# Optimization experiments

Hardware: AMD Instinct MI355X
Metric: run time of the kernel (lower is better)

Reference implementation:

```python
import jax, jax.numpy as jnp
import numpy as np
import math

H_SP, W_SP = 200, 200          # BEV spatial shape (single level, m == h)
D_MODEL = 256
N_HEADS = 8
N_POINTS = 4
D_HEAD = D_MODEL // N_HEADS


def _grid_init_bias():
    # Matches TemporalSelfAttention._reset_parameters for sampling_offsets.bias
    thetas = np.arange(N_HEADS, dtype=np.float32) * (2.0 * np.pi / N_HEADS)
    grid = np.stack([np.cos(thetas), np.sin(thetas)], -1)
    grid = grid / np.abs(grid).max(-1, keepdims=True)
    grid = np.tile(grid[:, None, None, :], (1, 1, N_POINTS, 1))  # (NH, 1, P, 2)
    for i in range(N_POINTS):
        grid[:, :, i, :] *= (i + 1)
    return jnp.asarray(grid.reshape(-1), dtype=jnp.float32)


def setup_inputs() -> dict:
    key = jax.random.key(0)
    ks = jax.random.split(key, 10)
    N = 1
    Lq = H_SP * W_SP
    Lin = H_SP * W_SP
    xav = math.sqrt(6.0 / (2 * D_MODEL))
    query = jax.random.normal(ks[0], (N, Lq, D_MODEL), jnp.float32)
    query_pos = jax.random.normal(ks[1], (N, Lq, D_MODEL), jnp.float32)
    reference_points = jax.random.uniform(ks[2], (N, Lq, 1, 2), jnp.float32)
    input_flatten = jax.random.normal(ks[3], (N, Lin, D_MODEL), jnp.float32)
    W_value = jax.random.uniform(ks[4], (D_MODEL, D_MODEL), jnp.float32, -xav, xav)
    b_value = jnp.zeros((D_MODEL,), jnp.float32)
    # small random weights (trained-model-like) + canonical grid bias
    W_off = jax.random.normal(ks[5], (N_HEADS * N_POINTS * 2, D_MODEL), jnp.float32) * 0.005
    b_off = _grid_init_bias()
    W_attn = jax.random.normal(ks[6], (N_HEADS * N_POINTS, D_MODEL), jnp.float32) * 0.02
    b_attn = jnp.zeros((N_HEADS * N_POINTS,), jnp.float32)
    W_out = jax.random.uniform(ks[7], (D_MODEL, D_MODEL), jnp.float32, -xav, xav)
    b_out = jnp.zeros((D_MODEL,), jnp.float32)
    return dict(query=query, query_pos=query_pos, reference_points=reference_points,
                input_flatten=input_flatten, W_value=W_value, b_value=b_value,
                W_off=W_off, b_off=b_off, W_attn=W_attn, b_attn=b_attn,
                W_out=W_out, b_out=b_out)


def _bilinear_sample(vflat, x, y):
    # vflat: (N, NH, H*W, DH); x, y: (N, NH, K) pixel coords (align_corners=False)
    # Zero padding outside the feature map, matching the MSDeformAttn CUDA kernel.
    x0f = jnp.floor(x)
    y0f = jnp.floor(y)
    x0 = x0f.astype(jnp.int32)
    y0 = y0f.astype(jnp.int32)
    lw = x - x0f
    lh = y - y0f
    gather = jax.vmap(jax.vmap(lambda v, i: v[i]))  # over batch, head
    acc = jnp.zeros(x.shape + (vflat.shape[-1],), vflat.dtype)
    corners = ((y0, x0, (1.0 - lh) * (1.0 - lw)),
               (y0, x0 + 1, (1.0 - lh) * lw),
               (y0 + 1, x0, lh * (1.0 - lw)),
               (y0 + 1, x0 + 1, lh * lw))
    for yi, xi, wgt in corners:
        valid = ((xi >= 0) & (xi < W_SP) & (yi >= 0) & (yi < H_SP)).astype(vflat.dtype)
        idx = jnp.clip(yi, 0, H_SP - 1) * W_SP + jnp.clip(xi, 0, W_SP - 1)
        g = gather(vflat, idx)                      # (N, NH, K, DH)
        acc = acc + (wgt * valid)[..., None] * g
    return acc


def reference(query, query_pos, reference_points, input_flatten,
              W_value, b_value, W_off, b_off, W_attn, b_attn, W_out, b_out):
    N, Lq, _ = query.shape
    q = query + query_pos
    value = input_flatten @ W_value.T + b_value                     # (N, Lin, D)
    value = value.reshape(N, -1, N_HEADS, D_HEAD).transpose(0, 2, 1, 3)  # (N, NH, Lin, DH)
    off = (q @ W_off.T + b_off).reshape(N, Lq, N_HEADS, N_POINTS, 2)
    attn = jax.nn.softmax((q @ W_attn.T + b_attn).reshape(N, Lq, N_HEADS, N_POINTS), axis=-1)
    norm = jnp.array([W_SP, H_SP], jnp.float32)                      # offset_normalizer (w, h)
    ref = reference_points[:, :, 0, :][:, :, None, None, :]          # (N, Lq, 1, 1, 2)
    loc = ref + off / norm                                           # (N, Lq, NH, P, 2) in [0,1]
    x = (loc[..., 0] * W_SP - 0.5).transpose(0, 2, 1, 3).reshape(N, N_HEADS, Lq * N_POINTS)
    y = (loc[..., 1] * H_SP - 0.5).transpose(0, 2, 1, 3).reshape(N, N_HEADS, Lq * N_POINTS)
    sampled = _bilinear_sample(value, x, y).reshape(N, N_HEADS, Lq, N_POINTS, D_HEAD)
    out = jnp.einsum('nhqpd,nqhp->nqhd', sampled, attn).reshape(N, Lq, D_MODEL)
    return out @ W_out.T + b_out
```

## Files before the change

kernel.cpp:

```cpp
#include <hip/hip_runtime.h>
#include <math.h>

#define LQ 40000
#define DMODEL 256
#define NHD 8
#define NPT 4
#define DHD 32
#define HSP 200
#define WSP 200
#define NSTRIP (LQ / 16)
#define G1B 128
#define G2B 256

typedef short s16x8 __attribute__((ext_vector_type(8)));
typedef float f32x4 __attribute__((ext_vector_type(4)));

__device__ __forceinline__ unsigned short f2b(float f) {
    unsigned u = __builtin_bit_cast(unsigned, f);
    u += 0x7FFFu + ((u >> 16) & 1u);
    return (unsigned short)(u >> 16);
}
__device__ __forceinline__ float b2f(unsigned short u) {
    return __builtin_bit_cast(float, ((unsigned)u) << 16);
}
__device__ __forceinline__ void pk8(const float4& v0, const float4& v1,
                                    unsigned short* o) {
    o[0] = f2b(v0.x); o[1] = f2b(v0.y); o[2] = f2b(v0.z); o[3] = f2b(v0.w);
    o[4] = f2b(v1.x); o[5] = f2b(v1.y); o[6] = f2b(v1.z); o[7] = f2b(v1.w);
}


__global__ __launch_bounds__(256) void convert_weights(
    const float* __restrict__ Wv, const float* __restrict__ Woff,
    const float* __restrict__ Wattn, const float* __restrict__ Wout,
    unsigned short* __restrict__ dst)
{
    int u = blockIdx.x * 256 + threadIdx.x;
    int lane = u & 63, ks = (u >> 6) & 7, slot = u >> 9;
    int l15 = lane & 15, quad = lane >> 4;
    const float* src;
    if (slot < 16) {
        src = Wv + (size_t)(slot * 16 + l15) * 256;
    } else if (slot < 22) {
        int col = (slot - 16) * 16 + l15;
        src = (col < 64) ? Woff + (size_t)col * 256
                         : Wattn + (size_t)(col - 64) * 256;
    } else {
        src = Wout + (size_t)((slot - 22) * 16 + l15) * 256;
    }
    int k0 = ks * 32 + quad * 8;
    float4 v0 = *(const float4*)(src + k0);
    float4 v1 = *(const float4*)(src + k0 + 4);
    union { unsigned short u16[8]; uint4 v; } tmp;
    pk8(v0, v1, tmp.u16);
    *(uint4*)(dst + (size_t)u * 8) = tmp.v;
}


__global__ __launch_bounds__(256, 2) void gemm12(
    const float* __restrict__ input_flatten,
    const float* __restrict__ query, const float* __restrict__ query_pos,
    const unsigned short* __restrict__ wf,
    const float* __restrict__ bv, const float* __restrict__ boff,
    const float* __restrict__ battn,
    unsigned short* __restrict__ val, float* __restrict__ raw2)
{
    __shared__ unsigned short Blds[32768];

    const int bid = blockIdx.x;
    const int t = threadIdx.x;
    const int role = (bid < 2 * G1B) ? 0 : 1;
    const int half8 = (bid >= G1B && role == 0) ? 1 : 0;

    {
        const uint4* src = (const uint4*)(wf + (role ? 16 : half8 * 8) * 4096);
        const int nu = role ? 3072 : 4096;
        for (int i = t; i < nu; i += 256) ((uint4*)Blds)[i] = src[i];
    }
    __syncthreads();

    const int wave = t >> 6, lane = t & 63;
    const int l15 = lane & 15, quad = lane >> 4;

    if (role == 0) {
        float bias[8];
#pragma unroll
        for (int c = 0; c < 8; ++c) bias[c] = bv[(half8 * 8 + c) * 16 + l15];
        const int wgid = (bid - half8 * G1B) * 4 + wave;
        for (int g = wgid; g < NSTRIP; g += G1B * 4) {
            const float* base = input_flatten + ((size_t)g * 16 + l15) * 256;
            float4 p0[8], p1[8];
#pragma unroll
            for (int ks = 0; ks < 8; ++ks) {
                p0[ks] = *(const float4*)(base + ks * 32 + quad * 8);
                p1[ks] = *(const float4*)(base + ks * 32 + quad * 8 + 4);
            }
            asm volatile("" ::: "memory");
            s16x8 a[8];
#pragma unroll
            for (int ks = 0; ks < 8; ++ks) {
                union { unsigned short u16[8]; s16x8 v; } tmp;
                pk8(p0[ks], p1[ks], tmp.u16);
                a[ks] = tmp.v;
            }
#pragma unroll
            for (int c = 0; c < 8; ++c) {
                const int gc = half8 * 8 + c;
                f32x4 acc = (f32x4){0.f, 0.f, 0.f, 0.f};
#pragma unroll
                for (int ks = 0; ks < 8; ++ks)
                    acc = __builtin_amdgcn_mfma_f32_16x16x32_bf16(
                        a[ks], *(const s16x8*)&Blds[c * 4096 + ks * 512 + lane * 8],
                        acc, 0, 0, 0);
#pragma unroll
                for (int r2 = 0; r2 < 4; ++r2) {
                    size_t row = (size_t)g * 16 + quad * 4 + r2;
                    val[(((size_t)(gc >> 1) * LQ + row) << 5) + ((gc & 1) << 4) + l15]
                        = f2b(acc[r2] + bias[c]);
                }
            }
        }
    } else {
        float bias[6];
#pragma unroll
        for (int c = 0; c < 6; ++c) {
            int col = c * 16 + l15;
            bias[c] = (col < 64) ? boff[col] : battn[col - 64];
        }
        const int wgid = (bid - 2 * G1B) * 4 + wave;
        for (int g = wgid; g < NSTRIP; g += G2B * 4) {
            const float* base  = query     + ((size_t)g * 16 + l15) * 256;
            const float* base2 = query_pos + ((size_t)g * 16 + l15) * 256;
            float4 p0[8], p1[8], q0[8], q1[8];
#pragma unroll
            for (int ks = 0; ks < 8; ++ks) {
                p0[ks] = *(const float4*)(base + ks * 32 + quad * 8);
                p1[ks] = *(const float4*)(base + ks * 32 + quad * 8 + 4);
                q0[ks] = *(const float4*)(base2 + ks * 32 + quad * 8);
                q1[ks] = *(const float4*)(base2 + ks * 32 + quad * 8 + 4);
            }
            asm volatile("" ::: "memory");
            s16x8 a[8];
#pragma unroll
            for (int ks = 0; ks < 8; ++ks) {
                float4 v0 = p0[ks], v1 = p1[ks];
                v0.x += q0[ks].x; v0.y += q0[ks].y;
                v0.z += q0[ks].z; v0.w += q0[ks].w;
                v1.x += q1[ks].x; v1.y += q1[ks].y;
                v1.z += q1[ks].z; v1.w += q1[ks].w;
                union { unsigned short u16[8]; s16x8 v; } tmp;
                pk8(v0, v1, tmp.u16);
                a[ks] = tmp.v;
            }
#pragma unroll
            for (int c = 0; c < 6; ++c) {
                f32x4 acc = (f32x4){0.f, 0.f, 0.f, 0.f};
#pragma unroll
                for (int ks = 0; ks < 8; ++ks)
                    acc = __builtin_amdgcn_mfma_f32_16x16x32_bf16(
                        a[ks], *(const s16x8*)&Blds[c * 4096 + ks * 512 + lane * 8],
                        acc, 0, 0, 0);
#pragma unroll
                for (int r2 = 0; r2 < 4; ++r2) {
                    size_t row = (size_t)g * 16 + quad * 4 + r2;
                    float v = acc[r2] + bias[c];
                    int col = c * 16 + l15;
                    int hh, jj;
                    if (col < 64) { hh = col >> 3; jj = col & 7; }
                    else          { hh = (col - 64) >> 2; jj = 8 + (col & 3); }
                    raw2[((size_t)hh * LQ + row) * 12 + jj] = v;
                }
            }
        }
    }
}

__global__ __launch_bounds__(256, 2) void gemm4(
    const unsigned short* __restrict__ Af, const unsigned short* __restrict__ wf,
    const float* __restrict__ bout, float* __restrict__ C)
{
    __shared__ unsigned short Blds[32768];

    const int t = threadIdx.x;
    const int half8 = blockIdx.x >> 7;
    {
        const uint4* src = (const uint4*)(wf + (22 + half8 * 8) * 4096);
        for (int i = t; i < 4096; i += 256) ((uint4*)Blds)[i] = src[i];
    }
    __syncthreads();

    const int wave = t >> 6, lane = t & 63;
    const int l15 = lane & 15, quad = lane >> 4;

    float bias[8];
#pragma unroll
    for (int c = 0; c < 8; ++c) bias[c] = bout[(half8 * 8 + c) * 16 + l15];

    const int wgid = (blockIdx.x & 127) * 4 + wave;
    for (int g = wgid; g < NSTRIP; g += 128 * 4) {
        s16x8 a[8];
#pragma unroll
        for (int ks = 0; ks < 8; ++ks)
            a[ks] = *(const s16x8*)&Af[(size_t)g * 4096 + ks * 512 + lane * 8];
        asm volatile("" ::: "memory");
#pragma unroll
        for (int c = 0; c < 8; ++c) {
            const int gc = half8 * 8 + c;
            f32x4 acc = (f32x4){0.f, 0.f, 0.f, 0.f};
#pragma unroll
            for (int ks = 0; ks < 8; ++ks)
                acc = __builtin_amdgcn_mfma_f32_16x16x32_bf16(
                    a[ks], *(const s16x8*)&Blds[c * 4096 + ks * 512 + lane * 8],
                    acc, 0, 0, 0);
#pragma unroll
            for (int r2 = 0; r2 < 4; ++r2) {
                size_t row = (size_t)g * 16 + quad * 4 + r2;
                C[row * 256 + gc * 16 + l15] = acc[r2] + bias[c];
            }
        }
    }
}

__global__ __launch_bounds__(256) void sample_kernel(
    const float* __restrict__ raw2, const float* __restrict__ rp,
    const unsigned short* __restrict__ value, unsigned short* __restrict__ outa)
{
    __shared__ int4   sIdx[64][4];
    __shared__ float4 sW[64][4];

    const int h = blockIdx.x & 7;
    const int q0 = (blockIdx.x >> 3) * 64;
    const int t = threadIdx.x;
    {
        const int qi = t >> 2, p = t & 3;
        const int q = q0 + qi;
        const float* r = raw2 + ((size_t)h * LQ + q) * 12;
        float l0 = r[8], l1 = r[9], l2 = r[10], l3 = r[11];
        float mx = fmaxf(fmaxf(l0, l1), fmaxf(l2, l3));
        float e0 = __expf(l0 - mx), e1 = __expf(l1 - mx);
        float e2 = __expf(l2 - mx), e3 = __expf(l3 - mx);
        float inv = 1.f / (e0 + e1 + e2 + e3);
        float ep = (p == 0) ? e0 : (p == 1) ? e1 : (p == 2) ? e2 : e3;
        float wp = ep * inv;

        float x = rp[(size_t)q * 2 + 0] * (float)WSP - 0.5f + r[p * 2 + 0];
        float y = rp[(size_t)q * 2 + 1] * (float)HSP - 0.5f + r[p * 2 + 1];
        float x0f = floorf(x), y0f = floorf(y);
        int x0 = (int)x0f, y0 = (int)y0f;
        float lw = x - x0f, lh = y - y0f;
        float cw[4] = {(1.f - lh) * (1.f - lw), (1.f - lh) * lw,
                       lh * (1.f - lw), lh * lw};
        int4 I; float4 W;
        int* Ip = &I.x; float* Wp = &W.x;
#pragma unroll
        for (int c = 0; c < 4; ++c) {
            int cx = x0 + (c & 1), cy = y0 + (c >> 1);
            bool valid = (cx >= 0) & (cx < WSP) & (cy >= 0) & (cy < HSP);
            int ccx = cx < 0 ? 0 : (cx > WSP - 1 ? WSP - 1 : cx);
            int ccy = cy < 0 ? 0 : (cy > HSP - 1 ? HSP - 1 : cy);
            Ip[c] = (ccy * WSP + ccx) * DHD;
            Wp[c] = valid ? cw[c] * wp : 0.f;
        }
        sIdx[qi][p] = I;
        sW[qi][p] = W;
    }
    __syncthreads();

    const int d8 = t & 7, qp = t >> 3;
    const unsigned short* vp = value + (size_t)h * LQ * DHD + d8 * 4;
#pragma unroll
    for (int e = 0; e < 2; ++e) {
        int qi = qp * 2 + e;
        float a0 = 0.f, a1 = 0.f, a2 = 0.f, a3 = 0.f;
#pragma unroll
        for (int p = 0; p < 4; ++p) {
            int4 I = sIdx[qi][p];
            float4 W = sW[qi][p];
            uint2 g0 = *(const uint2*)(vp + I.x);
            uint2 g1 = *(const uint2*)(vp + I.y);
            uint2 g2 = *(const uint2*)(vp + I.z);
            uint2 g3 = *(const uint2*)(vp + I.w);
            a0 += W.x * b2f((unsigned short)g0.x);
            a1 += W.x * b2f((unsigned short)(g0.x >> 16));
            a2 += W.x * b2f((unsigned short)g0.y);
            a3 += W.x * b2f((unsigned short)(g0.y >> 16));
            a0 += W.y * b2f((unsigned short)g1.x);
            a1 += W.y * b2f((unsigned short)(g1.x >> 16));
            a2 += W.y * b2f((unsigned short)g1.y);
            a3 += W.y * b2f((unsigned short)(g1.y >> 16));
            a0 += W.z * b2f((unsigned short)g2.x);
            a1 += W.z * b2f((unsigned short)(g2.x >> 16));
            a2 += W.z * b2f((unsigned short)g2.y);
            a3 += W.z * b2f((unsigned short)(g2.y >> 16));
            a0 += W.w * b2f((unsigned short)g3.x);
            a1 += W.w * b2f((unsigned short)(g3.x >> 16));
            a2 += W.w * b2f((unsigned short)g3.y);
            a3 += W.w * b2f((unsigned short)(g3.y >> 16));
        }
        int q = q0 + qi;
        size_t off = (size_t)(q >> 4) * 4096 + h * 512 + (d8 >> 1) * 128
                   + (q & 15) * 8 + (d8 & 1) * 4;
        union { unsigned short u16[4]; uint2 v; } o;
        o.u16[0] = f2b(a0); o.u16[1] = f2b(a1);
        o.u16[2] = f2b(a2); o.u16[3] = f2b(a3);
        *(uint2*)&outa[off] = o.v;
    }
}

extern "C" void kernel_launch(void* const* d_in, const int* in_sizes, int n_in,
                              void* d_out, int out_size, void* d_ws, size_t ws_size,
                              hipStream_t stream)
{
    const float* query         = (const float*)d_in[0];
    const float* query_pos     = (const float*)d_in[1];
    const float* ref_points    = (const float*)d_in[2];
    const float* input_flatten = (const float*)d_in[3];
    const float* W_value       = (const float*)d_in[4];
    const float* b_value       = (const float*)d_in[5];
    const float* W_off         = (const float*)d_in[6];
    const float* b_off         = (const float*)d_in[7];
    const float* W_attn        = (const float*)d_in[8];
    const float* b_attn        = (const float*)d_in[9];
    const float* W_out         = (const float*)d_in[10];
    const float* b_out         = (const float*)d_in[11];
    float* out = (float*)d_out;

    unsigned short* val  = (unsigned short*)d_ws;
    float*          raw2 = (float*)(val + (size_t)LQ * DMODEL);
    unsigned short* outa = (unsigned short*)(raw2 + (size_t)LQ * 96);
    unsigned short* wf   = outa + (size_t)LQ * DMODEL;

    dim3 blk(256);

    convert_weights<<<dim3(76), blk, 0, stream>>>(W_value, W_off, W_attn, W_out, wf);

    gemm12<<<dim3(2 * G1B + G2B), blk, 0, stream>>>(
        input_flatten, query, query_pos, wf,
        b_value, b_off, b_attn, val, raw2);

    sample_kernel<<<dim3(8 * (LQ / 64)), blk, 0, stream>>>(raw2, ref_points, val, outa);

    gemm4<<<dim3(256), blk, 0, stream>>>(outa, wf, b_out, out);
}
```

Before: 236.2 us.

## Use 1024-thread one-strip-per-wave blocks for projection GEMMs, dropping grid-stride loops

The value/offset/attention GEMM and the output GEMM now launch 1024-thread blocks, each wave handling exactly one 16-row strip instead of grid-striding over strips. This lets each block's LDS weight tile be shared by 16 waves and exposes more parallel waves to hide global-load latency. The query+query_pos loads in the second role are split into two halves to cut register pressure. In exchange, each block pays a larger weight-staging cost relative to its work, and the last blocks are partly idle.

```diff
diff --git a/kernel.cpp b/kernel.cpp
--- a/kernel.cpp
+++ b/kernel.cpp
@@ -9,8 +9,7 @@
 #define HSP 200
 #define WSP 200
 #define NSTRIP (LQ / 16)
-#define G1B 128
-#define G2B 256
+#define B1 157
 
 typedef short s16x8 __attribute__((ext_vector_type(8)));
 typedef float f32x4 __attribute__((ext_vector_type(4)));
@@ -57,7 +56,7 @@
 }
 
 
-__global__ __launch_bounds__(256, 2) void gemm12(
+__global__ __launch_bounds__(1024, 4) void gemm12(
     const float* __restrict__ input_flatten,
     const float* __restrict__ query, const float* __restrict__ query_pos,
     const unsigned short* __restrict__ wf,
@@ -69,13 +68,13 @@
 
     const int bid = blockIdx.x;
     const int t = threadIdx.x;
-    const int role = (bid < 2 * G1B) ? 0 : 1;
-    const int half8 = (bid >= G1B && role == 0) ? 1 : 0;
+    const int role = (bid < 2 * B1) ? 0 : 1;
+    const int half8 = (role == 0 && bid >= B1) ? 1 : 0;
 
     {
         const uint4* src = (const uint4*)(wf + (role ? 16 : half8 * 8) * 4096);
         const int nu = role ? 3072 : 4096;
-        for (int i = t; i < nu; i += 256) ((uint4*)Blds)[i] = src[i];
+        for (int i = t; i < nu; i += 1024) ((uint4*)Blds)[i] = src[i];
     }
     __syncthreads();
 
@@ -83,126 +82,26 @@
     const int l15 = lane & 15, quad = lane >> 4;
 
     if (role == 0) {
+        const int g = (bid - half8 * B1) * 16 + wave;
+        if (g >= NSTRIP) return;
         float bias[8];
 #pragma unroll
         for (int c = 0; c < 8; ++c) bias[c] = bv[(half8 * 8 + c) * 16 + l15];
-        const int wgid = (bid - half8 * G1B) * 4 + wave;
-        for (int g = wgid; g < NSTRIP; g += G1B * 4) {
-            const float* base = input_flatten + ((size_t)g * 16 + l15) * 256;
-            float4 p0[8], p1[8];
-#pragma unroll
-            for (int ks = 0; ks < 8; ++ks) {
-                p0[ks] = *(const float4*)(base + ks * 32 + quad * 8);
-                p1[ks] = *(const float4*)(base + ks * 32 + quad * 8 + 4);
-            }
-            asm volatile("" ::: "memory");
-            s16x8 a[8];
-#pragma unroll
-            for (int ks = 0; ks < 8; ++ks) {
-                union { unsigned short u16[8]; s16x8 v; } tmp;
-                pk8(p0[ks], p1[ks], tmp.u16);
-                a[ks] = tmp.v;
-            }
-#pragma unroll
-            for (int c = 0; c < 8; ++c) {
-                const int gc = half8 * 8 + c;
-                f32x4 acc = (f32x4){0.f, 0.f, 0.f, 0.f};
-#pragma unroll
-                for (int ks = 0; ks < 8; ++ks)
-                    acc = __builtin_amdgcn_mfma_f32_16x16x32_bf16(
-                        a[ks], *(const s16x8*)&Blds[c * 4096 + ks * 512 + lane * 8],
-                        acc, 0, 0, 0);
-#pragma unroll
-                for (int r2 = 0; r2 < 4; ++r2) {
-                    size_t row = (size_t)g * 16 + quad * 4 + r2;
-                    val[(((size_t)(gc >> 1) * LQ + row) << 5) + ((gc & 1) << 4) + l15]
-                        = f2b(acc[r2] + bias[c]);
-                }
-            }
-        }
-    } else {
-        float bias[6];
-#pragma unroll
-        for (int c = 0; c < 6; ++c) {
-            int col = c * 16 + l15;
-            bias[c] = (col < 64) ? boff[col] : battn[col - 64];
-        }
-        const int wgid = (bid - 2 * G1B) * 4 + wave;
-        for (int g = wgid; g < NSTRIP; g += G2B * 4) {
-            const float* base  = query     + ((size_t)g * 16 + l15) * 256;
-            const float* base2 = query_pos + ((size_t)g * 16 + l15) * 256;
-            float4 p0[8], p1[8], q0[8], q1[8];
-#pragma unroll
-            for (int ks = 0; ks < 8; ++ks) {
-                p0[ks] = *(const float4*)(base + ks * 32 + quad * 8);
-                p1[ks] = *(const float4*)(base + ks * 32 + quad * 8 + 4);
-                q0[ks] = *(const float4*)(base2 + ks * 32 + quad * 8);
-                q1[ks] = *(const float4*)(base2 + ks * 32 + quad * 8 + 4);
-            }
-            asm volatile("" ::: "memory");
-            s16x8 a[8];
-#pragma unroll
-            for (int ks = 0; ks < 8; ++ks) {
-                float4 v0 = p0[ks], v1 = p1[ks];
-                v0.x += q0[ks].x; v0.y += q0[ks].y;
-                v0.z += q0[ks].z; v0.w += q0[ks].w;
-                v1.x += q1[ks].x; v1.y += q1[ks].y;
-                v1.z += q1[ks].z; v1.w += q1[ks].w;
-                union { unsigned short u16[8]; s16x8 v; } tmp;
-                pk8(v0, v1, tmp.u16);
-                a[ks] = tmp.v;
-            }
-#pragma unroll
-            for (int c = 0; c < 6; ++c) {
-                f32x4 acc = (f32x4){0.f, 0.f, 0.f, 0.f};
-#pragma unroll
-                for (int ks = 0; ks < 8; ++ks)
-                    acc = __builtin_amdgcn_mfma_f32_16x16x32_bf16(
-                        a[ks], *(const s16x8*)&Blds[c * 4096 + ks * 512 + lane * 8],
-                        acc, 0, 0, 0);
-#pragma unroll
-                for (int r2 = 0; r2 < 4; ++r2) {
-                    size_t row = (size_t)g * 16 + quad * 4 + r2;
-                    float v = acc[r2] + bias[c];
-                    int col = c * 16 + l15;
-                    int hh, jj;
-                    if (col < 64) { hh = col >> 3; jj = col & 7; }
-                    else          { hh = (col - 64) >> 2; jj = 8 + (col & 3); }
-                    raw2[((size_t)hh * LQ + row) * 12 + jj] = v;
-                }
-            }
-        }
-    }
-}
-
-__global__ __launch_bounds__(256, 2) void gemm4(
-    const unsigned short* __restrict__ Af, const unsigned short* __restrict__ wf,
-    const float* __restrict__ bout, float* __restrict__ C)
-{
-    __shared__ unsigned short Blds[32768];
-
-    const int t = threadIdx.x;
-    const int half8 = blockIdx.x >> 7;
-    {
-        const uint4* src = (const uint4*)(wf + (22 + half8 * 8) * 4096);
-        for (int i = t; i < 4096; i += 256) ((uint4*)Blds)[i] = src[i];
-    }
-    __syncthreads();
-
-    const int wave = t >> 6, lane = t & 63;
-    const int l15 = lane & 15, quad = lane >> 4;
-
-    float bias[8];
-#pragma unroll
-    for (int c = 0; c < 8; ++c) bias[c] = bout[(half8 * 8 + c) * 16 + l15];
-
-    const int wgid = (blockIdx.x & 127) * 4 + wave;
-    for (int g = wgid; g < NSTRIP; g += 128 * 4) {
+        const float* base = input_flatten + ((size_t)g * 16 + l15) * 256;
+        float4 p0[8], p1[8];
+#pragma unroll
+        for (int ks = 0; ks < 8; ++ks) {
+            p0[ks] = *(const float4*)(base + ks * 32 + quad * 8);
+            p1[ks] = *(const float4*)(base + ks * 32 + quad * 8 + 4);
+        }
+        asm volatile("" ::: "memory");
         s16x8 a[8];
 #pragma unroll
-        for (int ks = 0; ks < 8; ++ks)
-            a[ks] = *(const s16x8*)&Af[(size_t)g * 4096 + ks * 512 + lane * 8];
-        asm volatile("" ::: "memory");
+        for (int ks = 0; ks < 8; ++ks) {
+            union { unsigned short u16[8]; s16x8 v; } tmp;
+            pk8(p0[ks], p1[ks], tmp.u16);
+            a[ks] = tmp.v;
+        }
 #pragma unroll
         for (int c = 0; c < 8; ++c) {
             const int gc = half8 * 8 + c;
@@ -215,8 +114,110 @@
 #pragma unroll
             for (int r2 = 0; r2 < 4; ++r2) {
                 size_t row = (size_t)g * 16 + quad * 4 + r2;
-                C[row * 256 + gc * 16 + l15] = acc[r2] + bias[c];
+                val[(((size_t)(gc >> 1) * LQ + row) << 5) + ((gc & 1) << 4) + l15]
+                    = f2b(acc[r2] + bias[c]);
             }
+        }
+    } else {
+        const int g = (bid - 2 * B1) * 16 + wave;
+        if (g >= NSTRIP) return;
+        float bias[6];
+#pragma unroll
+        for (int c = 0; c < 6; ++c) {
+            int col = c * 16 + l15;
+            bias[c] = (col < 64) ? boff[col] : battn[col - 64];
+        }
+        const float* base  = query     + ((size_t)g * 16 + l15) * 256;
+        const float* base2 = query_pos + ((size_t)g * 16 + l15) * 256;
+        s16x8 a[8];
+#pragma unroll
+        for (int h = 0; h < 2; ++h) {
+            float4 p0[4], p1[4], q0[4], q1[4];
+#pragma unroll
+            for (int i = 0; i < 4; ++i) {
+                const int k0 = (h * 4 + i) * 32 + quad * 8;
+                p0[i] = *(const float4*)(base + k0);
+                p1[i] = *(const float4*)(base + k0 + 4);
+                q0[i] = *(const float4*)(base2 + k0);
+                q1[i] = *(const float4*)(base2 + k0 + 4);
+            }
+            asm volatile("" ::: "memory");
+#pragma unroll
+            for (int i = 0; i < 4; ++i) {
+                float4 v0 = p0[i], v1 = p1[i];
+                v0.x += q0[i].x; v0.y += q0[i].y;
+                v0.z += q0[i].z; v0.w += q0[i].w;
+                v1.x += q1[i].x; v1.y += q1[i].y;
+                v1.z += q1[i].z; v1.w += q1[i].w;
+                union { unsigned short u16[8]; s16x8 v; } tmp;
+                pk8(v0, v1, tmp.u16);
+                a[h * 4 + i] = tmp.v;
+            }
+        }
+#pragma unroll
+        for (int c = 0; c < 6; ++c) {
+            f32x4 acc = (f32x4){0.f, 0.f, 0.f, 0.f};
+#pragma unroll
+            for (int ks = 0; ks < 8; ++ks)
+                acc = __builtin_amdgcn_mfma_f32_16x16x32_bf16(
+                    a[ks], *(const s16x8*)&Blds[c * 4096 + ks * 512 + lane * 8],
+                    acc, 0, 0, 0);
+#pragma unroll
+            for (int r2 = 0; r2 < 4; ++r2) {
+                size_t row = (size_t)g * 16 + quad * 4 + r2;
+                float v = acc[r2] + bias[c];
+                int col = c * 16 + l15;
+                int hh, jj;
+                if (col < 64) { hh = col >> 3; jj = col & 7; }
+                else          { hh = (col - 64) >> 2; jj = 8 + (col & 3); }
+                raw2[((size_t)hh * LQ + row) * 12 + jj] = v;
+            }
+        }
+    }
+}
+
+__global__ __launch_bounds__(1024, 4) void gemm4(
+    const unsigned short* __restrict__ Af, const unsigned short* __restrict__ wf,
+    const float* __restrict__ bout, float* __restrict__ C)
+{
+    __shared__ unsigned short Blds[32768];
+
+    const int t = threadIdx.x;
+    const int half8 = (blockIdx.x >= B1) ? 1 : 0;
+    {
+        const uint4* src = (const uint4*)(wf + (22 + half8 * 8) * 4096);
+        for (int i = t; i < 4096; i += 1024) ((uint4*)Blds)[i] = src[i];
+    }
+    __syncthreads();
+
+    const int wave = t >> 6, lane = t & 63;
+    const int l15 = lane & 15, quad = lane >> 4;
+
+    const int g = (blockIdx.x - half8 * B1) * 16 + wave;
+    if (g >= NSTRIP) return;
+
+    float bias[8];
+#pragma unroll
+    for (int c = 0; c < 8; ++c) bias[c] = bout[(half8 * 8 + c) * 16 + l15];
+
+    s16x8 a[8];
+#pragma unroll
+    for (int ks = 0; ks < 8; ++ks)
+        a[ks] = *(const s16x8*)&Af[(size_t)g * 4096 + ks * 512 + lane * 8];
+    asm volatile("" ::: "memory");
+#pragma unroll
+    for (int c = 0; c < 8; ++c) {
+        const int gc = half8 * 8 + c;
+        f32x4 acc = (f32x4){0.f, 0.f, 0.f, 0.f};
+#pragma unroll
+        for (int ks = 0; ks < 8; ++ks)
+            acc = __builtin_amdgcn_mfma_f32_16x16x32_bf16(
+                a[ks], *(const s16x8*)&Blds[c * 4096 + ks * 512 + lane * 8],
+                acc, 0, 0, 0);
+#pragma unroll
+        for (int r2 = 0; r2 < 4; ++r2) {
+            size_t row = (size_t)g * 16 + quad * 4 + r2;
+            C[row * 256 + gc * 16 + l15] = acc[r2] + bias[c];
         }
     }
 }
@@ -330,15 +331,15 @@
     unsigned short* outa = (unsigned short*)(raw2 + (size_t)LQ * 96);
     unsigned short* wf   = outa + (size_t)LQ * DMODEL;
 
-    dim3 blk(256);
-
-    convert_weights<<<dim3(76), blk, 0, stream>>>(W_value, W_off, W_attn, W_out, wf);
-
-    gemm12<<<dim3(2 * G1B + G2B), blk, 0, stream>>>(
+    convert_weights<<<dim3(76), dim3(256), 0, stream>>>(
+        W_value, W_off, W_attn, W_out, wf);
+
+    gemm12<<<dim3(3 * B1), dim3(1024), 0, stream>>>(
         input_flatten, query, query_pos, wf,
         b_value, b_off, b_attn, val, raw2);
 
-    sample_kernel<<<dim3(8 * (LQ / 64)), blk, 0, stream>>>(raw2, ref_points, val, outa);
-
-    gemm4<<<dim3(256), blk, 0, stream>>>(outa, wf, b_out, out);
-}
+    sample_kernel<<<dim3(8 * (LQ / 64)), dim3(256), 0, stream>>>(
+        raw2, ref_points, val, outa);
+
+    gemm4<<<dim3(2 * B1), dim3(1024), 0, stream>>>(outa, wf, b_out, out);
+}
```

Result: faster. 230.2 us (-2.5%).
